# Kernel optimization log

Hardware: AMD Instinct MI355X
Metric: run time of the kernel (lower is better)

Reference implementation:

```python
import jax, jax.numpy as jnp
import numpy as np

N = 2048   # nodes in the input graph
NB = 2048  # nodes in the barycenter graph
D = 128    # embedding (feature) dimension
K = 16     # number of atoms (len(size_atoms))


def cost_mat(cost_s, cost_t, p_s, p_t, tran, emb_s, emb_t):
    """Fused Gromov-Wasserstein cost matrix.

    GW structural part:  (C_s^2 p_s) 1^T + 1 (p_t^T (C_t^2)^T) - 2 C_s T C_t^T
    Fused feature part:  0.5 * squared Euclidean distance between node embeddings.
    """
    f1 = (cost_s ** 2) @ p_s                     # (N, 1)
    f2 = p_t.T @ (cost_t ** 2).T                 # (1, NB)
    cost = f1 + f2 - 2.0 * (cost_s @ tran) @ cost_t.T  # (N, NB)
    # pairwise squared Euclidean distances between embeddings
    d_emb = (jnp.sum(emb_s ** 2, axis=1, keepdims=True)
             + jnp.sum(emb_t ** 2, axis=1)[None, :]
             - 2.0 * emb_s @ emb_t.T)            # (N, NB)
    return cost + 0.5 * d_emb


def setup_inputs() -> dict:
    key = jax.random.key(0)
    k = jax.random.split(key, 6)
    graph = jax.random.uniform(k[0], (N, N), dtype=jnp.float32)
    embedding = jax.random.normal(k[1], (N, D), dtype=jnp.float32)
    prob = jnp.ones((N, 1), jnp.float32) / N           # uniform node distribution
    graph_b = jax.random.uniform(k[2], (NB, NB), dtype=jnp.float32)
    embedding_b = jax.random.normal(k[3], (NB, D), dtype=jnp.float32)
    prob_b = jnp.ones((NB, 1), jnp.float32) / NB
    t = jax.random.uniform(k[4], (N, NB), dtype=jnp.float32)
    tran = t / jnp.sum(t)                              # valid coupling-like plan (sums to 1)
    weights = jax.nn.softmax(jax.random.normal(k[5], (K,), dtype=jnp.float32))
    return {"graph": graph, "embedding": embedding, "prob": prob,
            "graph_b": graph_b, "embedding_b": embedding_b, "prob_b": prob_b,
            "tran": tran, "weights": weights, "ole_coeff": 1, "idx": 0}


def reference(graph, embedding, prob, graph_b, embedding_b, prob_b, tran, weights, ole_coeff, idx):
    # NOTE: the torch forward also computes cluster/entropy (OLE) losses from
    # `weights`, but they do NOT enter the returned value, which is only
    # <cost_mat(...), tran>. We therefore return exactly that inner product.
    cost = cost_mat(graph, graph_b, prob, prob_b, tran, embedding, embedding_b)
    return jnp.sum(cost * tran)
```

## Files before the change

### kernel.cpp

```cpp
#include <hip/hip_runtime.h>
#include <hip/hip_bf16.h>

#define NN 2048
#define DD 128

typedef unsigned short u16;
typedef unsigned int u32;
typedef __attribute__((ext_vector_type(8))) short bf16x8;
typedef __attribute__((ext_vector_type(4))) float f32x4;

__device__ __forceinline__ u16 f2bf(float f){
  u32 u = __float_as_uint(f);
  u32 r = (u + 0x7fffu + ((u >> 16) & 1u)) >> 16;
  return (u16)r;
}

__device__ __forceinline__ void gload16(const void* g, void* l){
  __builtin_amdgcn_global_load_lds(
      (const __attribute__((address_space(1))) u32*)g,
      (__attribute__((address_space(3))) u32*)l, 16, 0, 0);
}


__device__ __forceinline__ void rowpass_graph_body(
    int bid, int tid, const float* __restrict__ src, const float* __restrict__ w,
    u16* __restrict__ dst, float* __restrict__ red){
  int wid = tid >> 6, lane = tid & 63;
  int row = bid * 4 + wid;
  const float4* s4 = (const float4*)(src + (size_t)row * NN);
  float acc = 0.f;
  #pragma unroll
  for (int it = 0; it < NN / 256; ++it){
    int c4 = it * 64 + lane;
    float4 v = s4[c4];
    float4 ww = ((const float4*)w)[c4];
    acc += v.x*v.x*ww.x + v.y*v.y*ww.y + v.z*v.z*ww.z + v.w*v.w*ww.w;
    ushort4 o; o.x = f2bf(v.x); o.y = f2bf(v.y); o.z = f2bf(v.z); o.w = f2bf(v.w);
    ((ushort4*)(dst + (size_t)row * NN))[c4] = o;
  }
  #pragma unroll
  for (int off = 32; off; off >>= 1) acc += __shfl_down(acc, off);
  if (lane == 0) red[row] = acc;
}

__device__ __forceinline__ void tran_pass_body(
    int bx, int by, int t, float (*tile)[65],
    const float* __restrict__ src,
    u16* __restrict__ Tm, u16* __restrict__ Tt,
    float* __restrict__ rs, float* __restrict__ cls)
{
  int r0 = bx * 64, c0 = by * 64;
  #pragma unroll
  for (int it = 0; it < 4; ++it){
    int chunk = it * 256 + t; int r = chunk >> 4, c4 = chunk & 15;
    float4 v = ((const float4*)(src + (size_t)(r0 + r) * NN + c0))[c4];
    tile[r][c4*4+0] = v.x; tile[r][c4*4+1] = v.y;
    tile[r][c4*4+2] = v.z; tile[r][c4*4+3] = v.w;
    ushort4 o; o.x = f2bf(v.x); o.y = f2bf(v.y); o.z = f2bf(v.z); o.w = f2bf(v.w);
    ((ushort4*)(Tm + (size_t)(r0 + r) * NN + c0))[c4] = o;
  }
  __syncthreads();
  #pragma unroll
  for (int it = 0; it < 4; ++it){
    int chunk = it * 256 + t; int j = chunk >> 4, i4 = chunk & 15;
    ushort4 o;
    o.x = f2bf(tile[i4*4+0][j]); o.y = f2bf(tile[i4*4+1][j]);
    o.z = f2bf(tile[i4*4+2][j]); o.w = f2bf(tile[i4*4+3][j]);
    ((ushort4*)(Tt + (size_t)(c0 + j) * NN + r0))[i4] = o;
  }
  {
    int r = t >> 2, cq = (t & 3) * 16;
    float s = 0.f;
    #pragma unroll
    for (int c = 0; c < 16; ++c) s += tile[r][cq + c];
    s += __shfl_down(s, 2);
    s += __shfl_down(s, 1);
    if ((t & 3) == 0) atomicAdd(&rs[r0 + r], s);
  }
  {
    int c = t >> 2, rq = (t & 3) * 16;
    float s = 0.f;
    #pragma unroll
    for (int r = 0; r < 16; ++r) s += tile[rq + r][c];
    s += __shfl_down(s, 2);
    s += __shfl_down(s, 1);
    if ((t & 3) == 0) atomicAdd(&cls[c0 + c], s);
  }
}

__device__ __forceinline__ void graphb_pass_body(
    int bx, int by, int t, float (*tile)[65], float* pb,
    const float* __restrict__ src, const float* __restrict__ probb,
    u16* __restrict__ CtT, float* __restrict__ f2)
{
  int r0 = bx * 64, c0 = by * 64;
  if (t < 64) pb[t] = probb[c0 + t];
  #pragma unroll
  for (int it = 0; it < 4; ++it){
    int chunk = it * 256 + t; int r = chunk >> 4, c4 = chunk & 15;
    float4 v = ((const float4*)(src + (size_t)(r0 + r) * NN + c0))[c4];
    tile[r][c4*4+0] = v.x; tile[r][c4*4+1] = v.y;
    tile[r][c4*4+2] = v.z; tile[r][c4*4+3] = v.w;
  }
  __syncthreads();
  #pragma unroll
  for (int it = 0; it < 4; ++it){
    int chunk = it * 256 + t; int j = chunk >> 4, i4 = chunk & 15;
    ushort4 o;
    o.x = f2bf(tile[i4*4+0][j]); o.y = f2bf(tile[i4*4+1][j]);
    o.z = f2bf(tile[i4*4+2][j]); o.w = f2bf(tile[i4*4+3][j]);
    ((ushort4*)(CtT + (size_t)(c0 + j) * NN + r0))[i4] = o;
  }
  {
    int r = t >> 2, cq = (t & 3) * 16;
    float s = 0.f;
    #pragma unroll
    for (int c = 0; c < 16; ++c){ float v = tile[r][cq + c]; s += v * v * pb[cq + c]; }
    s += __shfl_down(s, 2);
    s += __shfl_down(s, 1);
    if ((t & 3) == 0) atomicAdd(&f2[r0 + r], s);
  }
}

__device__ __forceinline__ void emb_body(
    int bid, int t, const float* __restrict__ src, u16* __restrict__ dst,
    float* __restrict__ nrm){
  int rloc = t >> 5, lane32 = t & 31;
  int row = bid * 8 + rloc;
  float4 v = ((const float4*)(src + (size_t)row * DD))[lane32];
  float a = v.x*v.x + v.y*v.y + v.z*v.z + v.w*v.w;
  ushort4 o; o.x = f2bf(v.x); o.y = f2bf(v.y); o.z = f2bf(v.z); o.w = f2bf(v.w);
  ((ushort4*)(dst + (size_t)row * DD))[lane32] = o;
  #pragma unroll
  for (int off = 16; off; off >>= 1) a += __shfl_down(a, off, 32);
  if (lane32 == 0) nrm[row] = a;
}

__global__ __launch_bounds__(256) void k_prep(
    const float* __restrict__ graph,  const float* __restrict__ prob,
    const float* __restrict__ tran,   const float* __restrict__ graphb,
    const float* __restrict__ probb,  const float* __restrict__ emb,
    const float* __restrict__ embb,
    u16* Cs, u16* Tm, u16* Tt, u16* CtT, u16* es, u16* et,
    float* f1, float* f2, float* rs, float* cls, float* ss, float* st)
{
  __shared__ float tile[64][65];
  __shared__ float pb[64];
  int b = blockIdx.x, t = threadIdx.x;
  if (b < 512){
    rowpass_graph_body(b, t, graph, prob, Cs, f1);
  } else if (b < 1536){
    int b2 = b - 512;  tran_pass_body(b2 & 31, b2 >> 5, t, tile, tran, Tm, Tt, rs, cls);
  } else if (b < 2560){
    int b2 = b - 1536; graphb_pass_body(b2 & 31, b2 >> 5, t, tile, pb, graphb, probb, CtT, f2);
  } else if (b < 2816){
    emb_body(b - 2560, t, emb, es, ss);
  } else {
    emb_body(b - 2816, t, embb, et, st);
  }
}

__global__ __launch_bounds__(512, 2) void k_gw(
    const u16* __restrict__ Cs, const u16* __restrict__ Tt,
    const u16* __restrict__ Tm, const u16* __restrict__ CtT,
    float* __restrict__ accs)
{
  __shared__ u16 lds[2][4][8192];
  const int tid = threadIdx.x;
  const int bid = blockIdx.x;
  const int swz = (bid & 7) * 32 + (bid >> 3);
  const int bi = swz >> 4, bk = swz & 15;

  const u16* srcs[4] = {Cs, Tt, Tm, CtT};
  const int panels[4] = {bi * 128, bk * 128, bi * 128, bk * 128};

  const int w = tid >> 6, lane = tid & 63;
  const int l15 = lane & 15, g = lane >> 4;
  const int gsel = w >> 2, wg = w & 3, wr = wg >> 1, wc = wg & 1;

  const int s_row = tid >> 3;
  const int s_gslot = (tid & 7) ^ (s_row & 7);

  f32x4 acc[4][4];
  #pragma unroll
  for (int m = 0; m < 4; ++m)
    #pragma unroll
    for (int n = 0; n < 4; ++n)
      acc[m][n] = (f32x4){0.f, 0.f, 0.f, 0.f};

  int offA[4][2], offB[4][2];
  #pragma unroll
  for (int m = 0; m < 4; ++m){
    int row = wr * 64 + m * 16 + l15;
    int rowb = wc * 64 + m * 16 + l15;
    #pragma unroll
    for (int kk = 0; kk < 2; ++kk){
      offA[m][kk] = row * 64 + ((((kk << 2) | g)) ^ (row & 7)) * 8;
      offB[m][kk] = rowb * 64 + ((((kk << 2) | g)) ^ (rowb & 7)) * 8;
    }
  }

  auto stage = [&](int buf, int kt){
    const size_t col = (size_t)kt * 64 + s_gslot * 8;
    #pragma unroll
    for (int tt = 0; tt < 4; ++tt){
      gload16(srcs[tt] + (size_t)(panels[tt] + s_row) * NN + col,
              &lds[buf][tt][w * 512]);
      gload16(srcs[tt] + (size_t)(panels[tt] + s_row + 64) * NN + col,
              &lds[buf][tt][4096 + w * 512]);
    }
  };

  const int NT = NN / 64;
  stage(0, 0);
  stage(1, 1);
  for (int kt = 0; kt < NT; ++kt){
    int cur = kt & 1;
    asm volatile("s_waitcnt vmcnt(8)" ::: "memory");
    __builtin_amdgcn_s_barrier();

    const u16* tA = &lds[cur][gsel * 2][0];
    const u16* tB = &lds[cur][gsel * 2 + 1][0];
    bf16x8 av[4][2], bv[4][2];
    #pragma unroll
    for (int kk = 0; kk < 2; ++kk){
      #pragma unroll
      for (int m = 0; m < 4; ++m) av[m][kk] = *(const bf16x8*)(tA + offA[m][kk]);
      #pragma unroll
      for (int n = 0; n < 4; ++n) bv[n][kk] = *(const bf16x8*)(tB + offB[n][kk]);
    }
    asm volatile("s_waitcnt lgkmcnt(0)" ::: "memory");
    __builtin_amdgcn_sched_barrier(0);
    __builtin_amdgcn_s_barrier();

    int kn = (kt + 2 < NT) ? (kt + 2) : (NT - 1);
    stage(cur, kn);

    __builtin_amdgcn_s_setprio(1);
    #pragma unroll
    for (int kk = 0; kk < 2; ++kk)
      #pragma unroll
      for (int m = 0; m < 4; ++m)
        #pragma unroll
        for (int n = 0; n < 4; ++n)
          acc[m][n] = __builtin_amdgcn_mfma_f32_16x16x32_bf16(av[m][kk], bv[n][kk], acc[m][n], 0, 0, 0);
    __builtin_amdgcn_s_setprio(0);
  }

  __syncthreads();

  float* ustash = (float*)&lds[0][0][0];
  if (gsel == 0){
    #pragma unroll
    for (int m = 0; m < 4; ++m)
      #pragma unroll
      for (int n = 0; n < 4; ++n)
        #pragma unroll
        for (int r = 0; r < 4; ++r){
          int row = wr * 64 + m * 16 + g * 4 + r;
          int col = wc * 64 + n * 16 + l15;
          ustash[row * 128 + col] = acc[m][n][r];
        }
  }
  __syncthreads();
  if (gsel == 1){
    float part = 0.f;
    #pragma unroll
    for (int m = 0; m < 4; ++m)
      #pragma unroll
      for (int n = 0; n < 4; ++n)
        #pragma unroll
        for (int r = 0; r < 4; ++r){
          int row = wr * 64 + m * 16 + g * 4 + r;
          int col = wc * 64 + n * 16 + l15;
          part += acc[m][n][r] * ustash[row * 128 + col];
        }
    #pragma unroll
    for (int off = 32; off; off >>= 1) part += __shfl_down(part, off);
    if (lane == 0) atomicAdd(&accs[0], part);
  }
}

__global__ __launch_bounds__(256, 2) void k_embdot(
    const u16* __restrict__ es, const u16* __restrict__ et,
    const float* __restrict__ tran, float* __restrict__ accs)
{
  __shared__ u16 lds[2][16384];
  const int tid = threadIdx.x;
  const int bid = blockIdx.x;
  const int swz = (bid & 7) * 32 + (bid >> 3);
  const int bi = swz >> 4, bj = swz & 15;
  const int w = tid >> 6, lane = tid & 63;
  const int l15 = lane & 15, g = lane >> 4;
  const int wr = w >> 1, wc = w & 1;

  const u16* srcs[2] = {es, et};
  const int panels[2] = {bi * 128, bj * 128};

  #pragma unroll
  for (int tt = 0; tt < 2; ++tt){
    #pragma unroll
    for (int it = 0; it < 8; ++it){
      int chunk = w * 8 + it;
      int r = chunk * 4 + g;
      int s = l15 ^ (r & 15);
      gload16(srcs[tt] + (size_t)(panels[tt] + r) * DD + s * 8,
              &lds[tt][chunk * 512]);
    }
  }
  __syncthreads();

  f32x4 acc[4][4];
  #pragma unroll
  for (int m = 0; m < 4; ++m)
    #pragma unroll
    for (int n = 0; n < 4; ++n)
      acc[m][n] = (f32x4){0.f, 0.f, 0.f, 0.f};

  #pragma unroll
  for (int ks = 0; ks < 4; ++ks){
    bf16x8 av[4], bv[4];
    #pragma unroll
    for (int m = 0; m < 4; ++m){
      int row = wr * 64 + m * 16 + l15;
      int sp = (ks * 4 + g) ^ (row & 15);
      av[m] = *(const bf16x8*)((const char*)&lds[0][0] + row * 256 + sp * 16);
    }
    #pragma unroll
    for (int n = 0; n < 4; ++n){
      int rowb = wc * 64 + n * 16 + l15;
      int spb = (ks * 4 + g) ^ (rowb & 15);
      bv[n] = *(const bf16x8*)((const char*)&lds[1][0] + rowb * 256 + spb * 16);
    }
    #pragma unroll
    for (int m = 0; m < 4; ++m)
      #pragma unroll
      for (int n = 0; n < 4; ++n)
        acc[m][n] = __builtin_amdgcn_mfma_f32_16x16x32_bf16(av[m], bv[n], acc[m][n], 0, 0, 0);
  }

  float part = 0.f;
  #pragma unroll
  for (int m = 0; m < 4; ++m)
    #pragma unroll
    for (int n = 0; n < 4; ++n)
      #pragma unroll
      for (int r = 0; r < 4; ++r){
        int row = bi * 128 + wr * 64 + m * 16 + g * 4 + r;
        int col = bj * 128 + wc * 64 + n * 16 + l15;
        part += tran[(size_t)row * NN + col] * acc[m][n][r];
      }
  #pragma unroll
  for (int off = 32; off; off >>= 1) part += __shfl_down(part, off);
  if (lane == 0) atomicAdd(&accs[1], part);
}

__global__ void k_final(const float* __restrict__ f1, const float* __restrict__ f2,
                        const float* __restrict__ rowsum, const float* __restrict__ colsum,
                        const float* __restrict__ ss, const float* __restrict__ st,
                        const float* __restrict__ accs, float* out){
  __shared__ float red[256];
  int t = threadIdx.x;
  float part = 0.f;
  for (int i = t; i < NN; i += 256){
    part += (f1[i] + 0.5f * ss[i]) * rowsum[i];
    part += (f2[i] + 0.5f * st[i]) * colsum[i];
  }
  red[t] = part; __syncthreads();
  for (int s = 128; s; s >>= 1){ if (t < s) red[t] += red[t + s]; __syncthreads(); }
  if (t == 0){
    float total = red[0] - 2.0f * accs[0] - accs[1];
    out[0] = total;
  }
}

extern "C" void kernel_launch(void* const* d_in, const int* in_sizes, int n_in,
                              void* d_out, int out_size, void* d_ws, size_t ws_size,
                              hipStream_t stream)
{
  const float* graph  = (const float*)d_in[0];
  const float* emb    = (const float*)d_in[1];
  const float* prob   = (const float*)d_in[2];
  const float* graphb = (const float*)d_in[3];
  const float* embb   = (const float*)d_in[4];
  const float* probb  = (const float*)d_in[5];
  const float* tran   = (const float*)d_in[6];
  (void)in_sizes; (void)n_in; (void)out_size; (void)ws_size;

  char* ws = (char*)d_ws;
  u16* Cs   = (u16*)(ws + 0);
  u16* Tm   = (u16*)(ws + 8388608);
  u16* Tt   = (u16*)(ws + 16777216);
  u16* CtT  = (u16*)(ws + 25165824);
  u16* es   = (u16*)(ws + 33554432);
  u16* et   = (u16*)(ws + 34078720);
  float* f1   = (float*)(ws + 34603008);
  float* f2   = (float*)(ws + 34611200);
  float* rs   = (float*)(ws + 34619392);
  float* cls  = (float*)(ws + 34627584);
  float* ss   = (float*)(ws + 34635776);
  float* st   = (float*)(ws + 34643968);
  float* accs = (float*)(ws + 34652160);

  hipMemsetAsync(ws + 34603008, 0, 49216, stream);

  k_prep<<<3072, 256, 0, stream>>>(graph, prob, tran, graphb, probb, emb, embb,
                                   Cs, Tm, Tt, CtT, es, et,
                                   f1, f2, rs, cls, ss, st);
  k_gw<<<256, 512, 0, stream>>>(Cs, Tt, Tm, CtT, accs);
  k_embdot<<<256, 256, 0, stream>>>(es, et, tran, accs);
  k_final<<<1, 256, 0, stream>>>(f1, f2, rs, cls, ss, st, accs, (float*)d_out);
}
```

Measured before the change: 96.50 us.

## Load A operands directly from global into registers, halving LDS staging

The A-side tiles (Cs and Tm) are now read by each wave straight from global memory into registers, one k-step ahead and double-buffered in registers, rather than staged through LDS. Only the B-side tiles (Tt, CtT) still go through LDS, which halves the shared memory footprint and the LDS traffic. The vmcnt wait threshold is adjusted for the extra outstanding loads, and the setprio hints are dropped. The risk is less coalesced global reads, since each lane fetches 16 bytes from separate rows, and duplicate A reads across the waves that share a row block (wc=0/1), plus higher register pressure.

```diff
diff --git a/kernel.cpp b/kernel.cpp
--- a/kernel.cpp
+++ b/kernel.cpp
@@ -165,14 +165,12 @@
     const u16* __restrict__ Tm, const u16* __restrict__ CtT,
     float* __restrict__ accs)
 {
-  __shared__ u16 lds[2][4][8192];
+  __shared__ u16 lds[2][2][8192];
   const int tid = threadIdx.x;
   const int bid = blockIdx.x;
   const int swz = (bid & 7) * 32 + (bid >> 3);
   const int bi = swz >> 4, bk = swz & 15;
-
-  const u16* srcs[4] = {Cs, Tt, Tm, CtT};
-  const int panels[4] = {bi * 128, bk * 128, bi * 128, bk * 128};
+  const int biRow = bi * 128, bkRow = bk * 128;
 
   const int w = tid >> 6, lane = tid & 63;
   const int l15 = lane & 15, g = lane >> 4;
@@ -188,63 +186,76 @@
     for (int n = 0; n < 4; ++n)
       acc[m][n] = (f32x4){0.f, 0.f, 0.f, 0.f};
 
-  int offA[4][2], offB[4][2];
-  #pragma unroll
-  for (int m = 0; m < 4; ++m){
-    int row = wr * 64 + m * 16 + l15;
-    int rowb = wc * 64 + m * 16 + l15;
-    #pragma unroll
-    for (int kk = 0; kk < 2; ++kk){
-      offA[m][kk] = row * 64 + ((((kk << 2) | g)) ^ (row & 7)) * 8;
-      offB[m][kk] = rowb * 64 + ((((kk << 2) | g)) ^ (rowb & 7)) * 8;
-    }
-  }
-
-  auto stage = [&](int buf, int kt){
+  int offB[4][2];
+  #pragma unroll
+  for (int n = 0; n < 4; ++n){
+    int rowb = wc * 64 + n * 16 + l15;
+    #pragma unroll
+    for (int kk = 0; kk < 2; ++kk)
+      offB[n][kk] = rowb * 64 + ((((kk << 2) | g)) ^ (rowb & 7)) * 8;
+  }
+
+  const u16* Amat = gsel ? Tm : Cs;
+  const u16* aptr[4];
+  #pragma unroll
+  for (int m = 0; m < 4; ++m)
+    aptr[m] = Amat + (size_t)(biRow + wr * 64 + m * 16 + l15) * NN;
+
+  auto stageB = [&](int buf, int kt){
     const size_t col = (size_t)kt * 64 + s_gslot * 8;
-    #pragma unroll
-    for (int tt = 0; tt < 4; ++tt){
-      gload16(srcs[tt] + (size_t)(panels[tt] + s_row) * NN + col,
-              &lds[buf][tt][w * 512]);
-      gload16(srcs[tt] + (size_t)(panels[tt] + s_row + 64) * NN + col,
-              &lds[buf][tt][4096 + w * 512]);
-    }
+    gload16(Tt  + (size_t)(bkRow + s_row)      * NN + col, &lds[buf][0][w * 512]);
+    gload16(Tt  + (size_t)(bkRow + s_row + 64) * NN + col, &lds[buf][0][4096 + w * 512]);
+    gload16(CtT + (size_t)(bkRow + s_row)      * NN + col, &lds[buf][1][w * 512]);
+    gload16(CtT + (size_t)(bkRow + s_row + 64) * NN + col, &lds[buf][1][4096 + w * 512]);
   };
 
   const int NT = NN / 64;
-  stage(0, 0);
-  stage(1, 1);
-  for (int kt = 0; kt < NT; ++kt){
-    int cur = kt & 1;
-    asm volatile("s_waitcnt vmcnt(8)" ::: "memory");
+  bf16x8 avA[4][2], avB[4][2];
+
+  stageB(0, 0);
+  stageB(1, 1);
+  #pragma unroll
+  for (int m = 0; m < 4; ++m)
+    #pragma unroll
+    for (int kk = 0; kk < 2; ++kk)
+      avA[m][kk] = *(const bf16x8*)(aptr[m] + kk * 32 + g * 8);
+
+  auto body = [&](int kt, int cur, bf16x8 (&avc)[4][2], bf16x8 (&avn)[4][2]){
+    asm volatile("s_waitcnt vmcnt(12)" ::: "memory");
     __builtin_amdgcn_s_barrier();
 
-    const u16* tA = &lds[cur][gsel * 2][0];
-    const u16* tB = &lds[cur][gsel * 2 + 1][0];
-    bf16x8 av[4][2], bv[4][2];
-    #pragma unroll
-    for (int kk = 0; kk < 2; ++kk){
-      #pragma unroll
-      for (int m = 0; m < 4; ++m) av[m][kk] = *(const bf16x8*)(tA + offA[m][kk]);
+    const u16* tB = &lds[cur][gsel][0];
+    bf16x8 bv[4][2];
+    #pragma unroll
+    for (int kk = 0; kk < 2; ++kk)
       #pragma unroll
       for (int n = 0; n < 4; ++n) bv[n][kk] = *(const bf16x8*)(tB + offB[n][kk]);
-    }
     asm volatile("s_waitcnt lgkmcnt(0)" ::: "memory");
     __builtin_amdgcn_sched_barrier(0);
     __builtin_amdgcn_s_barrier();
 
-    int kn = (kt + 2 < NT) ? (kt + 2) : (NT - 1);
-    stage(cur, kn);
-
-    __builtin_amdgcn_s_setprio(1);
+    int ka = (kt + 1 < NT) ? (kt + 1) : (NT - 1);
+    #pragma unroll
+    for (int m = 0; m < 4; ++m)
+      #pragma unroll
+      for (int kk = 0; kk < 2; ++kk)
+        avn[m][kk] = *(const bf16x8*)(aptr[m] + (size_t)ka * 64 + kk * 32 + g * 8);
+
+    int kb = (kt + 2 < NT) ? (kt + 2) : (NT - 1);
+    stageB(cur, kb);
+
     #pragma unroll
     for (int kk = 0; kk < 2; ++kk)
       #pragma unroll
       for (int m = 0; m < 4; ++m)
         #pragma unroll
         for (int n = 0; n < 4; ++n)
-          acc[m][n] = __builtin_amdgcn_mfma_f32_16x16x32_bf16(av[m][kk], bv[n][kk], acc[m][n], 0, 0, 0);
-    __builtin_amdgcn_s_setprio(0);
+          acc[m][n] = __builtin_amdgcn_mfma_f32_16x16x32_bf16(avc[m][kk], bv[n][kk], acc[m][n], 0, 0, 0);
+  };
+
+  for (int kt = 0; kt < NT; kt += 2){
+    body(kt,     0, avA, avB);
+    body(kt + 1, 1, avB, avA);
   }
 
   __syncthreads();
```

New measurement: 139.8 us. 1.45x slower.
